# Kernel optimization log

Hardware: AMD Instinct MI355X
Metric: run time of the kernel (lower is better)

Reference implementation:

```python
import jax, jax.numpy as jnp
import numpy as np

K = 3  # torch_geometric knn_interpolate default
EPS = 1e-16


def knn_interpolate(l_y, l_pos, h_pos):
    # squared distances [N_h, N_l]
    d2 = jnp.sum((h_pos[:, None, :] - l_pos[None, :, :]) ** 2, axis=-1)
    neg_d, idx = jax.lax.top_k(-d2, K)          # k nearest: idx [N_h, K]
    w = 1.0 / jnp.maximum(-neg_d, EPS)           # inverse squared-distance weights
    feats = l_y[idx]                             # [N_h, K, F] gather
    return jnp.sum(w[..., None] * feats, axis=1) / jnp.sum(w, axis=1, keepdims=True)


def mlp(x, W1, b1, W2, b2, W3, b3):
    x = jax.nn.relu(x @ W1 + b1)
    x = jax.nn.relu(x @ W2 + b2)
    return x @ W3 + b3


def setup_inputs() -> dict:
    key = jax.random.key(0)
    ks = jax.random.split(key, 8)
    N_h, N_l, H, O = 32768, 8192, 512, 128
    s1 = 1.0 / np.sqrt(H)
    return {
        "emb": jax.random.normal(ks[0], (N_h, H), jnp.float32),
        "l_y": jax.random.normal(ks[1], (N_l, O), jnp.float32),
        "l_pos": jax.random.uniform(ks[2], (N_l, 3), jnp.float32),
        "h_pos": jax.random.uniform(ks[3], (N_h, 3), jnp.float32),
        "W1": jax.random.normal(ks[4], (H, H), jnp.float32) * s1,
        "b1": jnp.zeros((H,), jnp.float32),
        "W2": jax.random.normal(ks[5], (H, H), jnp.float32) * s1,
        "b2": jnp.zeros((H,), jnp.float32),
        "W3": jax.random.normal(ks[6], (H, O), jnp.float32) * s1,
        "b3": jnp.zeros((O,), jnp.float32),
    }


def reference(emb, l_y, l_pos, h_pos, W1, b1, W2, b2, W3, b3):
    x = mlp(emb, W1, b1, W2, b2, W3, b3)
    return x + knn_interpolate(l_y, l_pos, h_pos)
```

## Files before the change

### kernel.cpp

```cpp
#include <hip/hip_runtime.h>
#include <stdint.h>

typedef __attribute__((ext_vector_type(4))) float f32x4;
typedef __attribute__((ext_vector_type(8))) short bf16x8;
typedef __attribute__((ext_vector_type(4))) unsigned short u16x4;

#define AS1(p) ((const __attribute__((address_space(1))) void*)(p))
#define AS3(p) ((__attribute__((address_space(3))) void*)(p))

__device__ __forceinline__ unsigned short f2bf(float f){
  unsigned u = __builtin_bit_cast(unsigned, f);
  u += 0x7FFF + ((u >> 16) & 1);
  return (unsigned short)(u >> 16);
}

template<int N> __device__ __forceinline__ void waitcnt_vm(){
  if constexpr (N==0) asm volatile("s_waitcnt vmcnt(0)" ::: "memory");
  else if constexpr (N==2) asm volatile("s_waitcnt vmcnt(2)" ::: "memory");
  else if constexpr (N==3) asm volatile("s_waitcnt vmcnt(3)" ::: "memory");
  else if constexpr (N==4) asm volatile("s_waitcnt vmcnt(4)" ::: "memory");
  else if constexpr (N==6) asm volatile("s_waitcnt vmcnt(6)" ::: "memory");
}

__global__ __launch_bounds__(256) void k_transpose3(const float* __restrict__ W1,
                                                    const float* __restrict__ W2,
                                                    const float* __restrict__ W3,
                                                    unsigned short* __restrict__ W1t,
                                                    unsigned short* __restrict__ W2t,
                                                    unsigned short* __restrict__ W3t){
  const int z = blockIdx.z;
  const float* in; unsigned short* out; int R, C;
  if (z == 0){ in = W1; out = W1t; R = 512; C = 512; }
  else if (z == 1){ in = W2; out = W2t; R = 512; C = 512; }
  else { in = W3; out = W3t; R = 512; C = 128; if (blockIdx.x >= 4) return; }
  __shared__ float tile[32][33];
  int tx = threadIdx.x & 31, ty = threadIdx.x >> 5;
  int c0 = blockIdx.x*32, r0 = blockIdx.y*32;
  #pragma unroll
  for (int i = 0; i < 4; i++)
    tile[ty + i*8][tx] = in[(size_t)(r0 + ty + i*8)*C + c0 + tx];
  __syncthreads();
  #pragma unroll
  for (int i = 0; i < 4; i++)
    out[(size_t)(c0 + ty + i*8)*R + r0 + tx] = f2bf(tile[tx][ty + i*8]);
}

template<int BM, int NC, int TW, int MINW, bool AF32, bool RELU, bool OUTBF16, bool ADDOUT>
__global__ __launch_bounds__(TW, MINW) void k_gemm(const void* __restrict__ Av,
                                                   const unsigned short* __restrict__ Bt,
                                                   const float* __restrict__ bias,
                                                   void* __restrict__ out, int K){
  constexpr int WARPS_M = BM/64;
  constexpr int WARPS_N = (TW/64)/WARPS_M;
  constexpr int WN = NC/WARPS_N;
  constexpr int NI = WN/16;
  constexpr int IA = AF32 ? 0 : (BM*4)/TW;
  constexpr int IB = (NC*4)/TW;
  constexpr int LS = IA + IB;

  __shared__ short As[3][BM*32];
  __shared__ short Bs[3][NC*32];

  const int tid  = threadIdx.x;
  const int lane = tid & 63, wid = tid >> 6;
  const int wr = wid / WARPS_N, wc = wid % WARPS_N;
  const int l15 = lane & 15, lk = lane >> 4;
  const int bm = blockIdx.x, bn = blockIdx.y;

  const unsigned short* Bsrc[IB];
  #pragma unroll
  for (int q = 0; q < IB; q++){
    int row = q*(TW/4) + (tid >> 2);
    int ch  = (tid & 3) ^ ((row >> 1) & 3);
    Bsrc[q] = Bt + (size_t)bn*NC*K + (size_t)row*K + ch*8;
  }
  const unsigned short* Asrc16[IA > 0 ? IA : 1];
  if constexpr (!AF32){
    #pragma unroll
    for (int a = 0; a < IA; a++){
      int row = a*(TW/4) + (tid >> 2);
      int ch  = (tid & 3) ^ ((row >> 1) & 3);
      Asrc16[a] = (const unsigned short*)Av + (size_t)bm*BM*K + (size_t)row*K + ch*8;
    }
  }
  const float* A32 = (const float*)Av + (size_t)bm*BM*K + (size_t)(tid>>2)*K + (size_t)(tid&3)*8;
  const int woff = (tid >> 2)*32 + ((tid & 3) ^ (((tid >> 2) >> 1) & 3))*8;

#define STAGE_B(t_, bb_) do{ int k0_ = (t_) << 5; _Pragma("unroll") \
  for (int q = 0; q < IB; q++) \
    __builtin_amdgcn_global_load_lds(AS1(Bsrc[q] + k0_), AS3(&Bs[bb_][(q*(TW/4))*32 + tid*8]), 16, 0, 0); \
}while(0)
#define STAGE_A16(t_, bb_) do{ int k0_ = (t_) << 5; _Pragma("unroll") \
  for (int a = 0; a < IA; a++) \
    __builtin_amdgcn_global_load_lds(AS1(Asrc16[a] + k0_), AS3(&As[bb_][(a*(TW/4))*32 + tid*8]), 16, 0, 0); \
}while(0)
#define A_CONV_WRITE(bb_) do{ bf16x8 p_; _Pragma("unroll") \
  for (int j_ = 0; j_ < 4; j_++){ p_[j_] = (short)f2bf(ra0[j_]); p_[j_+4] = (short)f2bf(ra1[j_]); } \
  *(bf16x8*)&As[bb_][woff] = p_; \
}while(0)

  f32x4 acc[4][NI];
  #pragma unroll
  for (int i = 0; i < 4; i++)
    #pragma unroll
    for (int j = 0; j < NI; j++) acc[i][j] = (f32x4){0.f,0.f,0.f,0.f};

  const int nt = K >> 5;
  f32x4 ra0, ra1;

  if constexpr (AF32){
    ra0 = *(const f32x4*)(A32);
    ra1 = *(const f32x4*)(A32 + 4);
    STAGE_B(0, 0);
    STAGE_B(1, 1);
    waitcnt_vm<IB>();
    A_CONV_WRITE(0);
    asm volatile("s_waitcnt lgkmcnt(0)" ::: "memory");
  } else {
    STAGE_A16(0, 0); STAGE_B(0, 0);
    STAGE_A16(1, 1); STAGE_B(1, 1);
    waitcnt_vm<LS>();
  }
  __builtin_amdgcn_s_barrier();

  int b = 0;
  for (int t = 0; t < nt; ++t){
    bf16x8 af[4], bg[NI];
    #pragma unroll
    for (int i = 0; i < 4; i++){
      int R = wr*64 + i*16 + l15;
      af[i] = *(const bf16x8*)&As[b][R*32 + (lk ^ ((R >> 1) & 3))*8];
    }
    #pragma unroll
    for (int j = 0; j < NI; j++){
      int R = wc*WN + j*16 + l15;
      bg[j] = *(const bf16x8*)&Bs[b][R*32 + (lk ^ ((R >> 1) & 3))*8];
    }

    int b2 = b + 2; if (b2 >= 3) b2 -= 3;
    if constexpr (AF32){
      if (t + 1 < nt){
        int k1 = (t + 1) << 5;
        ra0 = *(const f32x4*)(A32 + k1);
        ra1 = *(const f32x4*)(A32 + k1 + 4);
      }
      if (t + 2 < nt) STAGE_B(t + 2, b2);
    } else {
      if (t + 2 < nt){ STAGE_A16(t + 2, b2); STAGE_B(t + 2, b2); }
    }

    __builtin_amdgcn_s_setprio(1);
    #pragma unroll
    for (int i = 0; i < 4; i++)
      #pragma unroll
      for (int j = 0; j < NI; j++)
        acc[i][j] = __builtin_amdgcn_mfma_f32_16x16x32_bf16(af[i], bg[j], acc[i][j], 0, 0, 0);
    __builtin_amdgcn_s_setprio(0);

    if (t + 2 < nt) waitcnt_vm<(AF32 ? IB : LS)>();
    else            waitcnt_vm<0>();
    if constexpr (AF32){
      if (t + 1 < nt){
        int wb = b + 1; if (wb >= 3) wb -= 3;
        A_CONV_WRITE(wb);
      }
    }
    asm volatile("s_waitcnt lgkmcnt(0)" ::: "memory");
    __builtin_amdgcn_s_barrier();
    b = (b + 1 == 3) ? 0 : b + 1;
  }
#undef STAGE_B
#undef STAGE_A16
#undef A_CONV_WRITE

  const int row0 = bm*BM + wr*64 + lk*4;
  const int col0 = bn*NC + wc*WN + l15;
  const int NOUT = NC*gridDim.y;
  #pragma unroll
  for (int i = 0; i < 4; i++){
    #pragma unroll
    for (int j = 0; j < NI; j++){
      int col = col0 + j*16;
      float bv = bias[col];
      #pragma unroll
      for (int r = 0; r < 4; r++){
        int row = row0 + i*16 + r;
        float v = acc[i][j][r] + bv;
        if (RELU) v = fmaxf(v, 0.f);
        if (ADDOUT) v = v + ((const float*)out)[(size_t)row*NOUT + col];
        if (OUTBF16) ((unsigned short*)out)[(size_t)row*NOUT + col] = f2bf(v);
        else         ((float*)out)[(size_t)row*NOUT + col] = v;
      }
    }
  }
}

#define GD 14
#define GD3 (GD*GD*GD)
#define NL 8192

__device__ __forceinline__ int cellcoord(float x){
  int c = (int)(x * (float)GD);
  return min(GD-1, max(0, c));
}

__global__ __launch_bounds__(64) void k_zero(int* __restrict__ p){
  #pragma unroll
  for (int i = 0; i < 16; i++)
    ((int4*)p)[threadIdx.x*16 + i] = (int4){0,0,0,0};
}

__global__ __launch_bounds__(256) void k_hist(const float* __restrict__ l_pos,
                                              int* __restrict__ hist){
  int i = blockIdx.x*256 + threadIdx.x;
  float x = l_pos[3*i], y = l_pos[3*i+1], z = l_pos[3*i+2];
  int c = (cellcoord(z)*GD + cellcoord(y))*GD + cellcoord(x);
  atomicAdd(&hist[c], 1);
}

__global__ __launch_bounds__(1024) void k_scan(const int* __restrict__ hist,
                                               int* __restrict__ cellStart,
                                               int* __restrict__ cursor){
  __shared__ int s[1024];
  int t = threadIdx.x;
  int4 v = ((const int4*)hist)[t];
  int sum = v.x + v.y + v.z + v.w;
  s[t] = sum;
  __syncthreads();
  for (int off = 1; off < 1024; off <<= 1){
    int val = (t >= off) ? s[t-off] : 0;
    __syncthreads();
    s[t] += val;
    __syncthreads();
  }
  int base = s[t] - sum;
  int4 cs;
  cs.x = base;
  cs.y = base + v.x;
  cs.z = base + v.x + v.y;
  cs.w = base + v.x + v.y + v.z;
  ((int4*)cellStart)[t] = cs;
  ((int4*)cursor)[t]    = cs;
}

__global__ __launch_bounds__(256) void k_scatter(const float* __restrict__ l_pos,
                                                 int* __restrict__ cursor,
                                                 float4* __restrict__ sorted){
  int i = blockIdx.x*256 + threadIdx.x;
  float x = l_pos[3*i], y = l_pos[3*i+1], z = l_pos[3*i+2];
  int c = (cellcoord(z)*GD + cellcoord(y))*GD + cellcoord(x);
  int slot = atomicAdd(&cursor[c], 1);
  float4 q; q.x = x; q.y = y; q.z = z; q.w = __int_as_float(i);
  sorted[slot] = q;
}

#define KNN_INS(dv, gi) \
  if (gi != i0 && gi != i1 && gi != i2 && \
      (dv < d2 || (dv == d2 && gi < i2))){ \
    if (dv < d1 || (dv == d1 && gi < i1)){ \
      d2 = d1; i2 = i1; \
      if (dv < d0 || (dv == d0 && gi < i0)){ d1 = d0; i1 = i0; d0 = dv; i0 = gi; } \
      else { d1 = dv; i1 = gi; } \
    } else { d2 = dv; i2 = gi; } \
  }

#define KNN_MERGE16() \
  _Pragma("unroll") \
  for (int m = 1; m < 16; m <<= 1){ \
    float e0 = __shfl_xor(d0, m), e1 = __shfl_xor(d1, m), e2 = __shfl_xor(d2, m); \
    int   j0 = __shfl_xor(i0, m), j1 = __shfl_xor(i1, m), j2 = __shfl_xor(i2, m); \
    KNN_INS(e0, j0); KNN_INS(e1, j1); KNN_INS(e2, j2); \
  }

__global__ __launch_bounds__(256) void k_knn_grid(const float* __restrict__ h_pos,
                                                  const int* __restrict__ cellStart,
                                                  const float4* __restrict__ sorted,
                                                  float* __restrict__ w,
                                                  int* __restrict__ idx){
  const int t = blockIdx.x*256 + threadIdx.x;
  const int h = t >> 4, sl = t & 15;
  const float hx = h_pos[3*h], hy = h_pos[3*h+1], hz = h_pos[3*h+2];
  const int cx = cellcoord(hx), cy = cellcoord(hy), cz = cellcoord(hz);
  const float cs = 1.0f/(float)GD;
  float d0 = 3e38f, d1 = 3e38f, d2 = 3e38f;
  int   i0 = 0x7fffffff, i1 = 0x7fffffff, i2 = 0x7fffffff;

  for (int ci = sl; ci < 27; ci += 16){
    int dz = ci/9 - 1, dy = (ci - (ci/9)*9)/3 - 1, dx = ci % 3 - 1;
    int zz = cz+dz, yy = cy+dy, xx = cx+dx;
    if ((unsigned)zz >= GD || (unsigned)yy >= GD || (unsigned)xx >= GD) continue;
    int c = (zz*GD + yy)*GD + xx;
    int p0 = cellStart[c], p1 = cellStart[c+1];
    for (int p = p0; p < p1; p++){
      float4 qq = sorted[p];
      float ddx = hx - qq.x, ddy = hy - qq.y, ddz = hz - qq.z;
      float d = fmaf(ddx, ddx, fmaf(ddy, ddy, ddz*ddz));
      int gi = __float_as_int(qq.w);
      KNN_INS(d, gi);
    }
  }
  KNN_MERGE16();

  for (int r = 2; r < GD; r++){
    int rp = r - 1;
    float B = 3e38f;
    if (cx - rp > 0)      B = fminf(B, hx - (float)(cx-rp)*cs);
    if (cx + rp + 1 < GD) B = fminf(B, (float)(cx+rp+1)*cs - hx);
    if (cy - rp > 0)      B = fminf(B, hy - (float)(cy-rp)*cs);
    if (cy + rp + 1 < GD) B = fminf(B, (float)(cy+rp+1)*cs - hy);
    if (cz - rp > 0)      B = fminf(B, hz - (float)(cz-rp)*cs);
    if (cz + rp + 1 < GD) B = fminf(B, (float)(cz+rp+1)*cs - hz);
    if (d2 <= B*B) break;

    int side = 2*r + 1, ss = side*side, tot = ss*side;
    for (int ci = sl; ci < tot; ci += 16){
      int dz = ci/ss - r;
      int rem = ci - (ci/ss)*ss;
      int dy = rem/side - r, dx = rem - (rem/side)*side - r;
      int adx = abs(dx), ady = abs(dy), adz = abs(dz);
      if (max(adx, max(ady, adz)) < r) continue;
      int zz = cz+dz, yy = cy+dy, xx = cx+dx;
      if ((unsigned)zz >= GD || (unsigned)yy >= GD || (unsigned)xx >= GD) continue;
      int c = (zz*GD + yy)*GD + xx;
      int p0 = cellStart[c], p1 = cellStart[c+1];
      for (int p = p0; p < p1; p++){
        float4 qq = sorted[p];
        float ddx = hx - qq.x, ddy = hy - qq.y, ddz = hz - qq.z;
        float d = fmaf(ddx, ddx, fmaf(ddy, ddy, ddz*ddz));
        int gi = __float_as_int(qq.w);
        KNN_INS(d, gi);
      }
    }
    KNN_MERGE16();
  }

  if (sl == 0){
    w[3*h+0] = 1.0f/fmaxf(d0, 1e-16f); idx[3*h+0] = i0;
    w[3*h+1] = 1.0f/fmaxf(d1, 1e-16f); idx[3*h+1] = i1;
    w[3*h+2] = 1.0f/fmaxf(d2, 1e-16f); idx[3*h+2] = i2;
  }
}

__global__ __launch_bounds__(256) void k_knn_gather(const float* __restrict__ w,
                                                    const int* __restrict__ idx,
                                                    const float* __restrict__ l_y,
                                                    float* __restrict__ out){
  const int t = blockIdx.x*256 + threadIdx.x;
  const int h = t >> 5, lane = t & 31;
  const float w0 = w[h*3+0], w1 = w[h*3+1], w2 = w[h*3+2];
  const int   j0 = idx[h*3+0], j1 = idx[h*3+1], j2 = idx[h*3+2];
  const f32x4* ly4 = (const f32x4*)l_y;
  f32x4 a = ly4[(size_t)j0*32 + lane]*w0
          + ly4[(size_t)j1*32 + lane]*w1
          + ly4[(size_t)j2*32 + lane]*w2;
  float inv = 1.0f/(w0 + w1 + w2);
  ((f32x4*)out)[(size_t)h*32 + lane] = a*inv;
}

extern "C" void kernel_launch(void* const* d_in, const int* in_sizes, int n_in,
                              void* d_out, int out_size, void* d_ws, size_t ws_size,
                              hipStream_t stream){
  const float* emb   = (const float*)d_in[0];
  const float* l_y   = (const float*)d_in[1];
  const float* l_pos = (const float*)d_in[2];
  const float* h_pos = (const float*)d_in[3];
  const float* W1    = (const float*)d_in[4];
  const float* b1    = (const float*)d_in[5];
  const float* W2    = (const float*)d_in[6];
  const float* b2    = (const float*)d_in[7];
  const float* W3    = (const float*)d_in[8];
  const float* b3    = (const float*)d_in[9];

  const int M = 32768, H = 512;

  char* ws = (char*)d_ws;
  unsigned short* bufA = (unsigned short*)(ws);
  unsigned short* bufB = (unsigned short*)(ws + 33554432);
  unsigned short* W1t  = (unsigned short*)(ws + 67108864);
  unsigned short* W2t  = (unsigned short*)(ws + 67633152);
  unsigned short* W3t  = (unsigned short*)(ws + 68157440);
  int*    hist      = (int*)   (ws + 68288512);
  int*    cellStart = (int*)   (ws + 68304896);
  int*    cursor    = (int*)   (ws + 68321280);
  float4* sorted    = (float4*)(ws + 68354048);
  float* wts = (float*)(ws + 74579968);
  int*   idx = (int*)  (ws + 74973184);

  k_transpose3<<<dim3(16, 16, 3), 256, 0, stream>>>(W1, W2, W3, W1t, W2t, W3t);

  k_zero<<<dim3(1), 64, 0, stream>>>(hist);
  k_hist<<<dim3(NL/256), 256, 0, stream>>>(l_pos, hist);
  k_scan<<<dim3(1), 1024, 0, stream>>>(hist, cellStart, cursor);
  k_scatter<<<dim3(NL/256), 256, 0, stream>>>(l_pos, cursor, sorted);
  k_knn_grid<<<dim3(M*16/256), 256, 0, stream>>>(h_pos, cellStart, sorted, wts, idx);
  k_knn_gather<<<dim3(M*32/256), 256, 0, stream>>>(wts, idx, l_y, (float*)d_out);

  k_gemm<128, 256, 512, 4, true,  true,  true,  false><<<dim3(M/128, 2), 512, 0, stream>>>(emb,  W1t, b1, bufB, H);
  k_gemm<128, 256, 512, 4, false, true,  true,  false><<<dim3(M/128, 2), 512, 0, stream>>>(bufB, W2t, b2, bufA, H);
  k_gemm<64,  128, 256, 2, false, false, false, true ><<<dim3(M/64,  1), 256, 0, stream>>>(bufA, W3t, b3, d_out, H);
}
```

Measured before the change: 120.0 us.

## Fuse preprocessing kernels, fuse kNN gather, retile GEMMs to BK=64 double-buffered

Merges the weight transpose with the grid build (histogram, scan, scatter in one shared-memory block) into a single launch. The kNN search now does the feature gather directly, dropping the weights and index buffers and one kernel. The GEMM kernel moves from a 32-wide K step with triple buffering to a 64-wide K step with double buffering, an 8-way XOR swizzle and 128x128 tiles with N-major grid ordering. The aim is fewer launches and fewer barriers per K. The risk is less load/compute overlap with only two stages and a serial single-block grid build.

```diff
diff --git a/kernel.cpp b/kernel.cpp
--- a/kernel.cpp
+++ b/kernel.cpp
@@ -3,7 +3,6 @@
 
 typedef __attribute__((ext_vector_type(4))) float f32x4;
 typedef __attribute__((ext_vector_type(8))) short bf16x8;
-typedef __attribute__((ext_vector_type(4))) unsigned short u16x4;
 
 #define AS1(p) ((const __attribute__((address_space(1))) void*)(p))
 #define AS3(p) ((__attribute__((address_space(3))) void*)(p))
@@ -16,19 +15,72 @@
 
 template<int N> __device__ __forceinline__ void waitcnt_vm(){
   if constexpr (N==0) asm volatile("s_waitcnt vmcnt(0)" ::: "memory");
-  else if constexpr (N==2) asm volatile("s_waitcnt vmcnt(2)" ::: "memory");
-  else if constexpr (N==3) asm volatile("s_waitcnt vmcnt(3)" ::: "memory");
   else if constexpr (N==4) asm volatile("s_waitcnt vmcnt(4)" ::: "memory");
-  else if constexpr (N==6) asm volatile("s_waitcnt vmcnt(6)" ::: "memory");
-}
-
-__global__ __launch_bounds__(256) void k_transpose3(const float* __restrict__ W1,
-                                                    const float* __restrict__ W2,
-                                                    const float* __restrict__ W3,
-                                                    unsigned short* __restrict__ W1t,
-                                                    unsigned short* __restrict__ W2t,
-                                                    unsigned short* __restrict__ W3t){
+}
+
+#define GD 14
+#define NL 8192
+
+__device__ __forceinline__ int cellcoord(float x){
+  int c = (int)(x * (float)GD);
+  return min(GD-1, max(0, c));
+}
+
+__global__ __launch_bounds__(256) void k_pre(const float* __restrict__ W1,
+                                             const float* __restrict__ W2,
+                                             const float* __restrict__ W3,
+                                             unsigned short* __restrict__ W1t,
+                                             unsigned short* __restrict__ W2t,
+                                             unsigned short* __restrict__ W3t,
+                                             const float* __restrict__ l_pos,
+                                             int* __restrict__ cellStart,
+                                             float4* __restrict__ sorted){
   const int z = blockIdx.z;
+  if (z == 3){
+    if (blockIdx.x != 0 || blockIdx.y != 0) return;
+    __shared__ int hist[4096];
+    __shared__ int cur[4096];
+    __shared__ int s[256];
+    const int t = threadIdx.x;
+    #pragma unroll
+    for (int k = 0; k < 16; k++) hist[k*256 + t] = 0;
+    __syncthreads();
+    for (int k = 0; k < 32; k++){
+      int i = k*256 + t;
+      float x = l_pos[3*i], y = l_pos[3*i+1], zz = l_pos[3*i+2];
+      int c = (cellcoord(zz)*GD + cellcoord(y))*GD + cellcoord(x);
+      atomicAdd(&hist[c], 1);
+    }
+    __syncthreads();
+    int loc[16]; int sum = 0;
+    #pragma unroll
+    for (int e = 0; e < 16; e++){ loc[e] = hist[t*16 + e]; sum += loc[e]; }
+    s[t] = sum;
+    __syncthreads();
+    for (int off = 1; off < 256; off <<= 1){
+      int val = (t >= off) ? s[t-off] : 0;
+      __syncthreads();
+      s[t] += val;
+      __syncthreads();
+    }
+    int base = s[t] - sum;
+    #pragma unroll
+    for (int e = 0; e < 16; e++){
+      cellStart[t*16 + e] = base;
+      cur[t*16 + e] = base;
+      base += loc[e];
+    }
+    __syncthreads();
+    for (int k = 0; k < 32; k++){
+      int i = k*256 + t;
+      float x = l_pos[3*i], y = l_pos[3*i+1], zz = l_pos[3*i+2];
+      int c = (cellcoord(zz)*GD + cellcoord(y))*GD + cellcoord(x);
+      int slot = atomicAdd(&cur[c], 1);
+      float4 q; q.x = x; q.y = y; q.z = zz; q.w = __int_as_float(i);
+      sorted[slot] = q;
+    }
+    return;
+  }
   const float* in; unsigned short* out; int R, C;
   if (z == 0){ in = W1; out = W1t; R = 512; C = 512; }
   else if (z == 1){ in = W2; out = W2t; R = 512; C = 512; }
@@ -45,58 +97,94 @@
     out[(size_t)(c0 + ty + i*8)*R + r0 + tx] = f2bf(tile[tx][ty + i*8]);
 }
 
-template<int BM, int NC, int TW, int MINW, bool AF32, bool RELU, bool OUTBF16, bool ADDOUT>
-__global__ __launch_bounds__(TW, MINW) void k_gemm(const void* __restrict__ Av,
-                                                   const unsigned short* __restrict__ Bt,
-                                                   const float* __restrict__ bias,
-                                                   void* __restrict__ out, int K){
+template<int BM, int NC, int TW, bool AF32, bool RELU, bool OUTBF16, bool ADDOUT>
+__global__ __launch_bounds__(TW, 2) void k_gemm64(const void* __restrict__ Av,
+                                                  const unsigned short* __restrict__ Bt,
+                                                  const float* __restrict__ bias,
+                                                  void* __restrict__ out,
+                                                  int K, int NOUT){
   constexpr int WARPS_M = BM/64;
   constexpr int WARPS_N = (TW/64)/WARPS_M;
   constexpr int WN = NC/WARPS_N;
   constexpr int NI = WN/16;
-  constexpr int IA = AF32 ? 0 : (BM*4)/TW;
-  constexpr int IB = (NC*4)/TW;
+  constexpr int IA = AF32 ? 0 : (BM*8)/TW;
+  constexpr int IAW = (BM*8)/TW;
+  constexpr int IB = (NC*8)/TW;
   constexpr int LS = IA + IB;
 
-  __shared__ short As[3][BM*32];
-  __shared__ short Bs[3][NC*32];
+  __shared__ short As[2][BM*64];
+  __shared__ short Bs[2][NC*64];
 
   const int tid  = threadIdx.x;
   const int lane = tid & 63, wid = tid >> 6;
   const int wr = wid / WARPS_N, wc = wid % WARPS_N;
   const int l15 = lane & 15, lk = lane >> 4;
-  const int bm = blockIdx.x, bn = blockIdx.y;
+  const int bn = blockIdx.x, bm = blockIdx.y;
 
   const unsigned short* Bsrc[IB];
+  int bdst[IB];
   #pragma unroll
   for (int q = 0; q < IB; q++){
-    int row = q*(TW/4) + (tid >> 2);
-    int ch  = (tid & 3) ^ ((row >> 1) & 3);
-    Bsrc[q] = Bt + (size_t)bn*NC*K + (size_t)row*K + ch*8;
-  }
-  const unsigned short* Asrc16[IA > 0 ? IA : 1];
+    int cp = q*TW + tid, r = cp >> 3, s8 = cp & 7;
+    int c  = s8 ^ (r & 7);
+    Bsrc[q] = Bt + (size_t)(bn*NC + r)*K + c*8;
+    bdst[q] = cp*8;
+  }
+  const unsigned short* Asrc[IA > 0 ? IA : 1];
+  int adst16[IA > 0 ? IA : 1];
   if constexpr (!AF32){
     #pragma unroll
-    for (int a = 0; a < IA; a++){
-      int row = a*(TW/4) + (tid >> 2);
-      int ch  = (tid & 3) ^ ((row >> 1) & 3);
-      Asrc16[a] = (const unsigned short*)Av + (size_t)bm*BM*K + (size_t)row*K + ch*8;
-    }
-  }
-  const float* A32 = (const float*)Av + (size_t)bm*BM*K + (size_t)(tid>>2)*K + (size_t)(tid&3)*8;
-  const int woff = (tid >> 2)*32 + ((tid & 3) ^ (((tid >> 2) >> 1) & 3))*8;
-
-#define STAGE_B(t_, bb_) do{ int k0_ = (t_) << 5; _Pragma("unroll") \
+    for (int q = 0; q < IA; q++){
+      int cp = q*TW + tid, r = cp >> 3, s8 = cp & 7;
+      int c  = s8 ^ (r & 7);
+      Asrc[q] = (const unsigned short*)Av + (size_t)(bm*BM + r)*K + c*8;
+      adst16[q] = cp*8;
+    }
+  }
+  const float* A32src[IAW];
+  int adstw[IAW];
+  if constexpr (AF32){
+    #pragma unroll
+    for (int w = 0; w < IAW; w++){
+      int cp = w*TW + tid, r = cp >> 3, s8 = cp & 7;
+      int c  = s8 ^ (r & 7);
+      A32src[w] = (const float*)Av + (size_t)(bm*BM + r)*K + c*8;
+      adstw[w] = cp*8;
+    }
+  }
+  int aoff[4][2], boff[NI][2];
+  #pragma unroll
+  for (int i = 0; i < 4; i++){
+    int R = wr*64 + i*16 + l15;
+    #pragma unroll
+    for (int kh = 0; kh < 2; kh++)
+      aoff[i][kh] = R*64 + ((kh*4 + lk) ^ (R & 7))*8;
+  }
+  #pragma unroll
+  for (int j = 0; j < NI; j++){
+    int R = wc*WN + j*16 + l15;
+    #pragma unroll
+    for (int kh = 0; kh < 2; kh++)
+      boff[j][kh] = R*64 + ((kh*4 + lk) ^ (R & 7))*8;
+  }
+
+#define STAGE_BF16(t_, bb_) do{ int k0_ = (t_) << 6; \
+  if constexpr (!AF32){ _Pragma("unroll") \
+    for (int q = 0; q < IA; q++) \
+      __builtin_amdgcn_global_load_lds(AS1(Asrc[q] + k0_), AS3(&As[bb_][adst16[q]]), 16, 0, 0); } \
+  _Pragma("unroll") \
   for (int q = 0; q < IB; q++) \
-    __builtin_amdgcn_global_load_lds(AS1(Bsrc[q] + k0_), AS3(&Bs[bb_][(q*(TW/4))*32 + tid*8]), 16, 0, 0); \
+    __builtin_amdgcn_global_load_lds(AS1(Bsrc[q] + k0_), AS3(&Bs[bb_][bdst[q]]), 16, 0, 0); \
 }while(0)
-#define STAGE_A16(t_, bb_) do{ int k0_ = (t_) << 5; _Pragma("unroll") \
-  for (int a = 0; a < IA; a++) \
-    __builtin_amdgcn_global_load_lds(AS1(Asrc16[a] + k0_), AS3(&As[bb_][(a*(TW/4))*32 + tid*8]), 16, 0, 0); \
+#define A_LOADS(t_) do{ int k0_ = (t_) << 6; _Pragma("unroll") \
+  for (int w = 0; w < IAW; w++){ \
+    ra[w][0] = *(const f32x4*)(A32src[w] + k0_); \
+    ra[w][1] = *(const f32x4*)(A32src[w] + k0_ + 4); } \
 }while(0)
-#define A_CONV_WRITE(bb_) do{ bf16x8 p_; _Pragma("unroll") \
-  for (int j_ = 0; j_ < 4; j_++){ p_[j_] = (short)f2bf(ra0[j_]); p_[j_+4] = (short)f2bf(ra1[j_]); } \
-  *(bf16x8*)&As[bb_][woff] = p_; \
+#define A_CONV_WRITE(bb_) do{ _Pragma("unroll") \
+  for (int w = 0; w < IAW; w++){ bf16x8 p_; _Pragma("unroll") \
+    for (int j_ = 0; j_ < 4; j_++){ p_[j_] = (short)f2bf(ra[w][0][j_]); p_[j_+4] = (short)f2bf(ra[w][1][j_]); } \
+    *(bf16x8*)&As[bb_][adstw[w]] = p_; } \
 }while(0)
 
   f32x4 acc[4][NI];
@@ -105,77 +193,67 @@
     #pragma unroll
     for (int j = 0; j < NI; j++) acc[i][j] = (f32x4){0.f,0.f,0.f,0.f};
 
-  const int nt = K >> 5;
-  f32x4 ra0, ra1;
+  const int nt = K >> 6;
+  f32x4 ra[AF32 ? IAW : 1][2];
 
   if constexpr (AF32){
-    ra0 = *(const f32x4*)(A32);
-    ra1 = *(const f32x4*)(A32 + 4);
-    STAGE_B(0, 0);
-    STAGE_B(1, 1);
-    waitcnt_vm<IB>();
+    A_LOADS(0);
+    STAGE_BF16(0, 0);
+    waitcnt_vm<4>();
     A_CONV_WRITE(0);
-    asm volatile("s_waitcnt lgkmcnt(0)" ::: "memory");
   } else {
-    STAGE_A16(0, 0); STAGE_B(0, 0);
-    STAGE_A16(1, 1); STAGE_B(1, 1);
-    waitcnt_vm<LS>();
-  }
+    STAGE_BF16(0, 0);
+  }
+  waitcnt_vm<0>();
+  asm volatile("s_waitcnt lgkmcnt(0)" ::: "memory");
   __builtin_amdgcn_s_barrier();
 
   int b = 0;
   for (int t = 0; t < nt; ++t){
-    bf16x8 af[4], bg[NI];
-    #pragma unroll
-    for (int i = 0; i < 4; i++){
-      int R = wr*64 + i*16 + l15;
-      af[i] = *(const bf16x8*)&As[b][R*32 + (lk ^ ((R >> 1) & 3))*8];
-    }
-    #pragma unroll
-    for (int j = 0; j < NI; j++){
-      int R = wc*WN + j*16 + l15;
-      bg[j] = *(const bf16x8*)&Bs[b][R*32 + (lk ^ ((R >> 1) & 3))*8];
-    }
-
-    int b2 = b + 2; if (b2 >= 3) b2 -= 3;
-    if constexpr (AF32){
-      if (t + 1 < nt){
-        int k1 = (t + 1) << 5;
-        ra0 = *(const f32x4*)(A32 + k1);
-        ra1 = *(const f32x4*)(A32 + k1 + 4);
-      }
-      if (t + 2 < nt) STAGE_B(t + 2, b2);
-    } else {
-      if (t + 2 < nt){ STAGE_A16(t + 2, b2); STAGE_B(t + 2, b2); }
-    }
-
-    __builtin_amdgcn_s_setprio(1);
+    bf16x8 af[4][2], bg[NI][2];
     #pragma unroll
     for (int i = 0; i < 4; i++)
       #pragma unroll
-      for (int j = 0; j < NI; j++)
-        acc[i][j] = __builtin_amdgcn_mfma_f32_16x16x32_bf16(af[i], bg[j], acc[i][j], 0, 0, 0);
+      for (int kh = 0; kh < 2; kh++)
+        af[i][kh] = *(const bf16x8*)&As[b][aoff[i][kh]];
+    #pragma unroll
+    for (int j = 0; j < NI; j++)
+      #pragma unroll
+      for (int kh = 0; kh < 2; kh++)
+        bg[j][kh] = *(const bf16x8*)&Bs[b][boff[j][kh]];
+
+    if (t + 1 < nt){
+      if constexpr (AF32){ A_LOADS(t + 1); }
+      STAGE_BF16(t + 1, b ^ 1);
+    }
+
+    __builtin_amdgcn_s_setprio(1);
+    #pragma unroll
+    for (int kh = 0; kh < 2; kh++)
+      #pragma unroll
+      for (int i = 0; i < 4; i++)
+        #pragma unroll
+        for (int j = 0; j < NI; j++)
+          acc[i][j] = __builtin_amdgcn_mfma_f32_16x16x32_bf16(af[i][kh], bg[j][kh], acc[i][j], 0, 0, 0);
     __builtin_amdgcn_s_setprio(0);
 
-    if (t + 2 < nt) waitcnt_vm<(AF32 ? IB : LS)>();
-    else            waitcnt_vm<0>();
-    if constexpr (AF32){
-      if (t + 1 < nt){
-        int wb = b + 1; if (wb >= 3) wb -= 3;
-        A_CONV_WRITE(wb);
+    if (t + 1 < nt){
+      if constexpr (AF32){
+        waitcnt_vm<4>();
+        A_CONV_WRITE(b ^ 1);
       }
+      waitcnt_vm<0>();
     }
     asm volatile("s_waitcnt lgkmcnt(0)" ::: "memory");
     __builtin_amdgcn_s_barrier();
-    b = (b + 1 == 3) ? 0 : b + 1;
-  }
-#undef STAGE_B
-#undef STAGE_A16
+    b ^= 1;
+  }
+#undef STAGE_BF16
+#undef A_LOADS
 #undef A_CONV_WRITE
 
   const int row0 = bm*BM + wr*64 + lk*4;
   const int col0 = bn*NC + wc*WN + l15;
-  const int NOUT = NC*gridDim.y;
   #pragma unroll
   for (int i = 0; i < 4; i++){
     #pragma unroll
@@ -195,65 +273,6 @@
   }
 }
 
-#define GD 14
-#define GD3 (GD*GD*GD)
-#define NL 8192
-
-__device__ __forceinline__ int cellcoord(float x){
-  int c = (int)(x * (float)GD);
-  return min(GD-1, max(0, c));
-}
-
-__global__ __launch_bounds__(64) void k_zero(int* __restrict__ p){
-  #pragma unroll
-  for (int i = 0; i < 16; i++)
-    ((int4*)p)[threadIdx.x*16 + i] = (int4){0,0,0,0};
-}
-
-__global__ __launch_bounds__(256) void k_hist(const float* __restrict__ l_pos,
-                                              int* __restrict__ hist){
-  int i = blockIdx.x*256 + threadIdx.x;
-  float x = l_pos[3*i], y = l_pos[3*i+1], z = l_pos[3*i+2];
-  int c = (cellcoord(z)*GD + cellcoord(y))*GD + cellcoord(x);
-  atomicAdd(&hist[c], 1);
-}
-
-__global__ __launch_bounds__(1024) void k_scan(const int* __restrict__ hist,
-                                               int* __restrict__ cellStart,
-                                               int* __restrict__ cursor){
-  __shared__ int s[1024];
-  int t = threadIdx.x;
-  int4 v = ((const int4*)hist)[t];
-  int sum = v.x + v.y + v.z + v.w;
-  s[t] = sum;
-  __syncthreads();
-  for (int off = 1; off < 1024; off <<= 1){
-    int val = (t >= off) ? s[t-off] : 0;
-    __syncthreads();
-    s[t] += val;
-    __syncthreads();
-  }
-  int base = s[t] - sum;
-  int4 cs;
-  cs.x = base;
-  cs.y = base + v.x;
-  cs.z = base + v.x + v.y;
-  cs.w = base + v.x + v.y + v.z;
-  ((int4*)cellStart)[t] = cs;
-  ((int4*)cursor)[t]    = cs;
-}
-
-__global__ __launch_bounds__(256) void k_scatter(const float* __restrict__ l_pos,
-                                                 int* __restrict__ cursor,
-                                                 float4* __restrict__ sorted){
-  int i = blockIdx.x*256 + threadIdx.x;
-  float x = l_pos[3*i], y = l_pos[3*i+1], z = l_pos[3*i+2];
-  int c = (cellcoord(z)*GD + cellcoord(y))*GD + cellcoord(x);
-  int slot = atomicAdd(&cursor[c], 1);
-  float4 q; q.x = x; q.y = y; q.z = z; q.w = __int_as_float(i);
-  sorted[slot] = q;
-}
-
 #define KNN_INS(dv, gi) \
   if (gi != i0 && gi != i1 && gi != i2 && \
       (dv < d2 || (dv == d2 && gi < i2))){ \
@@ -272,11 +291,11 @@
     KNN_INS(e0, j0); KNN_INS(e1, j1); KNN_INS(e2, j2); \
   }
 
-__global__ __launch_bounds__(256) void k_knn_grid(const float* __restrict__ h_pos,
-                                                  const int* __restrict__ cellStart,
-                                                  const float4* __restrict__ sorted,
-                                                  float* __restrict__ w,
-                                                  int* __restrict__ idx){
+__global__ __launch_bounds__(256) void k_knn(const float* __restrict__ h_pos,
+                                             const int* __restrict__ cellStart,
+                                             const float4* __restrict__ sorted,
+                                             const float* __restrict__ l_y,
+                                             float* __restrict__ out){
   const int t = blockIdx.x*256 + threadIdx.x;
   const int h = t >> 4, sl = t & 15;
   const float hx = h_pos[3*h], hy = h_pos[3*h+1], hz = h_pos[3*h+2];
@@ -334,27 +353,19 @@
     KNN_MERGE16();
   }
 
-  if (sl == 0){
-    w[3*h+0] = 1.0f/fmaxf(d0, 1e-16f); idx[3*h+0] = i0;
-    w[3*h+1] = 1.0f/fmaxf(d1, 1e-16f); idx[3*h+1] = i1;
-    w[3*h+2] = 1.0f/fmaxf(d2, 1e-16f); idx[3*h+2] = i2;
-  }
-}
-
-__global__ __launch_bounds__(256) void k_knn_gather(const float* __restrict__ w,
-                                                    const int* __restrict__ idx,
-                                                    const float* __restrict__ l_y,
-                                                    float* __restrict__ out){
-  const int t = blockIdx.x*256 + threadIdx.x;
-  const int h = t >> 5, lane = t & 31;
-  const float w0 = w[h*3+0], w1 = w[h*3+1], w2 = w[h*3+2];
-  const int   j0 = idx[h*3+0], j1 = idx[h*3+1], j2 = idx[h*3+2];
+  float w0 = 1.0f/fmaxf(d0, 1e-16f);
+  float w1 = 1.0f/fmaxf(d1, 1e-16f);
+  float w2 = 1.0f/fmaxf(d2, 1e-16f);
+  float inv = 1.0f/(w0 + w1 + w2);
   const f32x4* ly4 = (const f32x4*)l_y;
-  f32x4 a = ly4[(size_t)j0*32 + lane]*w0
-          + ly4[(size_t)j1*32 + lane]*w1
-          + ly4[(size_t)j2*32 + lane]*w2;
-  float inv = 1.0f/(w0 + w1 + w2);
-  ((f32x4*)out)[(size_t)h*32 + lane] = a*inv;
+  size_t b0 = (size_t)i0*32 + sl*2;
+  size_t b1 = (size_t)i1*32 + sl*2;
+  size_t b2 = (size_t)i2*32 + sl*2;
+  f32x4 a0 = ly4[b0]*w0     + ly4[b1]*w1     + ly4[b2]*w2;
+  f32x4 a1 = ly4[b0 + 1]*w0 + ly4[b1 + 1]*w1 + ly4[b2 + 1]*w2;
+  size_t o = (size_t)h*32 + sl*2;
+  ((f32x4*)out)[o]     = a0*inv;
+  ((f32x4*)out)[o + 1] = a1*inv;
 }
 
 extern "C" void kernel_launch(void* const* d_in, const int* in_sizes, int n_in,
@@ -379,23 +390,15 @@
   unsigned short* W1t  = (unsigned short*)(ws + 67108864);
   unsigned short* W2t  = (unsigned short*)(ws + 67633152);
   unsigned short* W3t  = (unsigned short*)(ws + 68157440);
-  int*    hist      = (int*)   (ws + 68288512);
   int*    cellStart = (int*)   (ws + 68304896);
-  int*    cursor    = (int*)   (ws + 68321280);
   float4* sorted    = (float4*)(ws + 68354048);
-  float* wts = (float*)(ws + 74579968);
-  int*   idx = (int*)  (ws + 74973184);
-
-  k_transpose3<<<dim3(16, 16, 3), 256, 0, stream>>>(W1, W2, W3, W1t, W2t, W3t);
-
-  k_zero<<<dim3(1), 64, 0, stream>>>(hist);
-  k_hist<<<dim3(NL/256), 256, 0, stream>>>(l_pos, hist);
-  k_scan<<<dim3(1), 1024, 0, stream>>>(hist, cellStart, cursor);
-  k_scatter<<<dim3(NL/256), 256, 0, stream>>>(l_pos, cursor, sorted);
-  k_knn_grid<<<dim3(M*16/256), 256, 0, stream>>>(h_pos, cellStart, sorted, wts, idx);
-  k_knn_gather<<<dim3(M*32/256), 256, 0, stream>>>(wts, idx, l_y, (float*)d_out);
-
-  k_gemm<128, 256, 512, 4, true,  true,  true,  false><<<dim3(M/128, 2), 512, 0, stream>>>(emb,  W1t, b1, bufB, H);
-  k_gemm<128, 256, 512, 4, false, true,  true,  false><<<dim3(M/128, 2), 512, 0, stream>>>(bufB, W2t, b2, bufA, H);
-  k_gemm<64,  128, 256, 2, false, false, false, true ><<<dim3(M/64,  1), 256, 0, stream>>>(bufA, W3t, b3, d_out, H);
-}
+
+  k_pre<<<dim3(16, 16, 4), 256, 0, stream>>>(W1, W2, W3, W1t, W2t, W3t,
+                                             l_pos, cellStart, sorted);
+
+  k_knn<<<dim3(M*16/256), 256, 0, stream>>>(h_pos, cellStart, sorted, l_y, (float*)d_out);
+
+  k_gemm64<128, 128, 256, true,  true,  true,  false><<<dim3(4, M/128), 256, 0, stream>>>(emb,  W1t, b1, bufB, H, 512);
+  k_gemm64<128, 128, 256, false, true,  true,  false><<<dim3(4, M/128), 256, 0, stream>>>(bufB, W2t, b2, bufA, H, 512);
+  k_gemm64<64,  128, 256, false, false, false, true ><<<dim3(1, M/64),  256, 0, stream>>>(bufA, W3t, b3, d_out, H, 128);
+}
```

Result: slower. 145.2 us (+20.9%).
